# Optimization experiments

Hardware: AMD Instinct MI355X
Metric: run time of the kernel (lower is better)

The kernel has to match this reference:

```python
import jax, jax.numpy as jnp
import numpy as np

H = 768      # hidden_size
R = 64       # lora_dim
E = 8        # n_experts
B, S = 8, 2048


def setup_inputs() -> dict:
    key = jax.random.key(0)
    ks = jax.random.split(key, 10)
    s_in = 1.0 / np.sqrt(H)
    s_r = 1.0 / np.sqrt(R)
    return {
        "x": jax.random.normal(ks[0], (B, S, H), dtype=jnp.float32),
        "enc_w": jax.random.uniform(ks[1], (H, R), jnp.float32, -s_in, s_in),
        "enc_b": jax.random.uniform(ks[2], (R,), jnp.float32, -s_in, s_in),
        "sw_w": jax.random.uniform(ks[3], (R, E), jnp.float32, -s_r, s_r),
        "sw_b": jax.random.uniform(ks[4], (E,), jnp.float32, -s_r, s_r),
        "w1": jax.random.uniform(ks[5], (E, H, R), jnp.float32, -s_in, s_in),
        "b1": jax.random.uniform(ks[6], (E, R), jnp.float32, -s_in, s_in),
        "w2": jax.random.uniform(ks[7], (E, R, H), jnp.float32, -s_r, s_r),
        "b2": jax.random.uniform(ks[8], (E, H), jnp.float32, -s_r, s_r),
    }


def reference(x, enc_w, enc_b, sw_w, sw_b, w1, b1, w2, b2):
    b, s, d = x.shape
    xt = x.reshape(-1, d)                                  # [T, H]
    # router: encoder -> switch -> softmax -> top-1
    x_enc = xt @ enc_w + enc_b                             # [T, R]
    route_prob = jax.nn.softmax(x_enc @ sw_w + sw_b, axis=-1)  # [T, E]
    route_prob_max = jnp.max(route_prob, axis=-1)          # [T]
    routes = jnp.argmax(route_prob, axis=-1)               # [T]
    onehot = jax.nn.one_hot(routes, E, dtype=xt.dtype)     # [T, E]
    # dense dispatch: per-(token, expert) LoRA bottleneck; masked combine
    h = jnp.einsum('td,edr->ter', xt, w1) + b1[None]       # [T, E, R]
    h = jax.nn.gelu(h, approximate=False)
    h = h * onehot[..., None]                              # zero non-routed
    out = jnp.einsum('ter,erd->td', h, w2) + onehot @ b2   # [T, H]
    out = out * route_prob_max[:, None]
    return out.reshape(b, s, d)
```

## Files before the change

kernel.cpp:

```cpp
#include <hip/hip_runtime.h>
#include <math.h>

#define HDIM 768
#define RDIM 64
#define NEXP 8
#define NTOK 16384

typedef _Float16 half8 __attribute__((ext_vector_type(8)));
typedef float float4_t __attribute__((ext_vector_type(4)));

__device__ __forceinline__ float gelu_exact(float v) {
    return 0.5f * v * (1.0f + erff(v * 0.70710678118654752440f));
}

__global__ __launch_bounds__(256) void prep_kernel(
    const float* __restrict__ w1, const float* __restrict__ w2,
    const float* __restrict__ enc_w,
    _Float16* __restrict__ w1t, _Float16* __restrict__ w2t,
    _Float16* __restrict__ enc_hi, _Float16* __restrict__ enc_lo)
{
    const int wid = blockIdx.x * 4 + (threadIdx.x >> 6);
    const int lane = threadIdx.x & 63;
    if (wid < 768) {
        const int e = wid / 96, k0 = (wid % 96) * 8;
        half8 o;
        #pragma unroll
        for (int j = 0; j < 8; j++)
            o[j] = (_Float16)w1[((size_t)(e * HDIM + k0 + j)) * RDIM + lane];
        *(half8*)(w1t + ((size_t)(e * RDIM + lane)) * HDIM + k0) = o;
    } else if (wid < 1536) {
        const int id = wid - 768;
        const int e = id / 96, rem = id % 96;
        const int n = (rem >> 3) * 64 + lane, k0 = (rem & 7) * 8;
        half8 o;
        #pragma unroll
        for (int j = 0; j < 8; j++)
            o[j] = (_Float16)w2[((size_t)(e * RDIM + k0 + j)) * HDIM + n];
        *(half8*)(w2t + ((size_t)(e * HDIM + n)) * RDIM + k0) = o;
    } else if (wid < 1632) {
        const int k0 = (wid - 1536) * 8;
        half8 hi, lo;
        #pragma unroll
        for (int j = 0; j < 8; j++) {
            float v = enc_w[(size_t)(k0 + j) * RDIM + lane];
            _Float16 h = (_Float16)v;
            hi[j] = h;
            lo[j] = (_Float16)(v - (float)h);
        }
        *(half8*)(enc_hi + (size_t)lane * HDIM + k0) = hi;
        *(half8*)(enc_lo + (size_t)lane * HDIM + k0) = lo;
    }
}

__global__ __launch_bounds__(256) void router_kernel(
    const float* __restrict__ x,
    const _Float16* __restrict__ enc_hi, const _Float16* __restrict__ enc_lo,
    const float* __restrict__ enc_b, const float* __restrict__ sw_w,
    const float* __restrict__ sw_b, float* __restrict__ pmax,
    int* __restrict__ counts, int* __restrict__ lists)
{
    __shared__ __align__(16) float xe[64][68];
    __shared__ __align__(16) float sws[512];
    __shared__ int lcnt[NEXP], gbase[NEXP];

    const int tid = threadIdx.x;
    const int tok0 = blockIdx.x * 64;
    const int wv = tid >> 6, lane = tid & 63;
    const int q = lane >> 4, c = lane & 15;

    if (tid < 128) ((float4*)sws)[tid] = ((const float4*)sw_w)[tid];
    if (tid < NEXP) lcnt[tid] = 0;

    const float* xrow = x + (size_t)(tok0 + wv * 16 + c) * HDIM;
    const _Float16* ebase_hi = enc_hi + (size_t)c * HDIM + q * 8;
    const _Float16* ebase_lo = enc_lo + (size_t)c * HDIM + q * 8;

    float4_t acc[4] = {{0,0,0,0},{0,0,0,0},{0,0,0,0},{0,0,0,0}};
    #pragma unroll 2
    for (int k0 = 0; k0 < HDIM; k0 += 32) {
        float4 u0 = *(const float4*)(xrow + k0 + q * 8);
        float4 u1 = *(const float4*)(xrow + k0 + q * 8 + 4);
        float u[8] = {u0.x, u0.y, u0.z, u0.w, u1.x, u1.y, u1.z, u1.w};
        half8 ah, al;
        #pragma unroll
        for (int j = 0; j < 8; j++) {
            _Float16 h = (_Float16)u[j];
            ah[j] = h;
            al[j] = (_Float16)(u[j] - (float)h);
        }
        #pragma unroll
        for (int nf = 0; nf < 4; nf++) {
            half8 bh = *(const half8*)(ebase_hi + (size_t)nf * 16 * HDIM + k0);
            half8 bl = *(const half8*)(ebase_lo + (size_t)nf * 16 * HDIM + k0);
            acc[nf] = __builtin_amdgcn_mfma_f32_16x16x32_f16(ah, bh, acc[nf], 0, 0, 0);
            acc[nf] = __builtin_amdgcn_mfma_f32_16x16x32_f16(ah, bl, acc[nf], 0, 0, 0);
            acc[nf] = __builtin_amdgcn_mfma_f32_16x16x32_f16(al, bh, acc[nf], 0, 0, 0);
        }
    }

    {
        float ebv[4];
        #pragma unroll
        for (int nf = 0; nf < 4; nf++) ebv[nf] = enc_b[nf * 16 + c];
        #pragma unroll
        for (int nf = 0; nf < 4; nf++)
            #pragma unroll
            for (int i = 0; i < 4; i++)
                xe[wv * 16 + q * 4 + i][nf * 16 + c] = acc[nf][i] + ebv[nf];
    }
    __syncthreads();

    int amr[2], lpr[2];
    const int e = tid & 7;
    #pragma unroll
    for (int pass = 0; pass < 2; pass++) {
        const int t = (tid >> 3) + 32 * pass;
        float logit = sw_b[e];
        #pragma unroll 16
        for (int r = 0; r < RDIM; r++)
            logit += xe[t][r] * sws[r * NEXP + e];
        float m = logit; int am = e;
        #pragma unroll
        for (int d = 4; d >= 1; d >>= 1) {
            float om = __shfl_xor(m, d, 8);
            int oam  = __shfl_xor(am, d, 8);
            if (om > m || (om == m && oam < am)) { m = om; am = oam; }
        }
        float s = expf(logit - m);
        #pragma unroll
        for (int d = 1; d <= 4; d <<= 1) s += __shfl_xor(s, d, 8);
        amr[pass] = am; lpr[pass] = 0;
        if (e == 0) {
            pmax[tok0 + t] = 1.0f / s;
            lpr[pass] = atomicAdd(&lcnt[am], 1);
        }
    }
    __syncthreads();
    if (tid < NEXP) gbase[tid] = atomicAdd(&counts[tid * 32], lcnt[tid]);
    __syncthreads();
    if (e == 0) {
        #pragma unroll
        for (int pass = 0; pass < 2; pass++) {
            const int t = (tid >> 3) + 32 * pass;
            lists[amr[pass] * NTOK + gbase[amr[pass]] + lpr[pass]] = tok0 + t;
        }
    }
}

__global__ __launch_bounds__(256) void mm1_kernel(
    const float* __restrict__ x, const _Float16* __restrict__ w1t,
    const float* __restrict__ b1, const int* __restrict__ counts,
    const int* __restrict__ lists, _Float16* __restrict__ h)
{
    const int e = blockIdx.x;
    const int cnt = counts[e * 32];
    const int wv = threadIdx.x >> 6, lane = threadIdx.x & 63;
    const int q = lane >> 4, c = lane & 15;

    for (int st = blockIdx.y * 4 + wv; st * 16 < cnt; st += 512) {
        const int base = st * 16;
        const int nt = cnt - base;
        const int tA = lists[e * NTOK + base + min(c, nt - 1)];
        const float* xrow = x + (size_t)tA * HDIM;
        const _Float16* wbase = w1t + ((size_t)(e * RDIM + c)) * HDIM + q * 8;

        float4_t acc[4] = {{0,0,0,0},{0,0,0,0},{0,0,0,0},{0,0,0,0}};
        #pragma unroll 4
        for (int k0 = 0; k0 < HDIM; k0 += 32) {
            float4 u0 = *(const float4*)(xrow + k0 + q * 8);
            float4 u1 = *(const float4*)(xrow + k0 + q * 8 + 4);
            half8 a;
            a[0] = (_Float16)u0.x; a[1] = (_Float16)u0.y;
            a[2] = (_Float16)u0.z; a[3] = (_Float16)u0.w;
            a[4] = (_Float16)u1.x; a[5] = (_Float16)u1.y;
            a[6] = (_Float16)u1.z; a[7] = (_Float16)u1.w;
            #pragma unroll
            for (int nf = 0; nf < 4; nf++) {
                half8 b = *(const half8*)(wbase + (size_t)nf * 16 * HDIM + k0);
                acc[nf] = __builtin_amdgcn_mfma_f32_16x16x32_f16(a, b, acc[nf], 0, 0, 0);
            }
        }

        #pragma unroll
        for (int i = 0; i < 4; i++) {
            const int row = q * 4 + i;
            if (row < nt) {
                const int tok = lists[e * NTOK + base + row];
                _Float16* hrow = h + (size_t)tok * RDIM;
                #pragma unroll
                for (int nf = 0; nf < 4; nf++) {
                    float v = acc[nf][i] + b1[e * RDIM + nf * 16 + c];
                    hrow[nf * 16 + c] = (_Float16)gelu_exact(v);
                }
            }
        }
    }
}

__global__ __launch_bounds__(256) void mm2_kernel(
    const _Float16* __restrict__ h, const _Float16* __restrict__ w2t,
    const float* __restrict__ b2, const float* __restrict__ pmax,
    const int* __restrict__ counts, const int* __restrict__ lists,
    float* __restrict__ out)
{
    const int e = blockIdx.x;
    const int cnt = counts[e * 32];
    const int wv = threadIdx.x >> 6, lane = threadIdx.x & 63;
    const int q = lane >> 4, c = lane & 15;

    const int task = blockIdx.y * 4 + wv;
    const int nch = task % 3;
    const int sidx = task / 3;

    for (int st = sidx; st * 16 < cnt; st += 128) {
        const int base = st * 16;
        const int nt = cnt - base;
        const int tA = lists[e * NTOK + base + min(c, nt - 1)];
        half8 a0 = *(const half8*)(h + (size_t)tA * RDIM + q * 8);
        half8 a1 = *(const half8*)(h + (size_t)tA * RDIM + 32 + q * 8);

        int tokv[4]; float pm[4]; bool ok[4];
        #pragma unroll
        for (int i = 0; i < 4; i++) {
            const int row = q * 4 + i;
            ok[i] = row < nt;
            tokv[i] = lists[e * NTOK + base + min(row, nt - 1)];
            pm[i] = pmax[tokv[i]];
        }

        #pragma unroll 4
        for (int nf = 0; nf < 16; nf++) {
            const int n = nch * 256 + nf * 16 + c;
            const _Float16* wrow = w2t + ((size_t)(e * HDIM + n)) * RDIM;
            half8 b0 = *(const half8*)(wrow + q * 8);
            half8 b1v = *(const half8*)(wrow + 32 + q * 8);
            float4_t acc = {0, 0, 0, 0};
            acc = __builtin_amdgcn_mfma_f32_16x16x32_f16(a0, b0, acc, 0, 0, 0);
            acc = __builtin_amdgcn_mfma_f32_16x16x32_f16(a1, b1v, acc, 0, 0, 0);
            const float b2v = b2[e * HDIM + n];
            #pragma unroll
            for (int i = 0; i < 4; i++) {
                if (ok[i])
                    out[(size_t)tokv[i] * HDIM + n] = (acc[i] + b2v) * pm[i];
            }
        }
    }
}

extern "C" void kernel_launch(void* const* d_in, const int* in_sizes, int n_in,
                              void* d_out, int out_size, void* d_ws, size_t ws_size,
                              hipStream_t stream) {
    const float* x     = (const float*)d_in[0];
    const float* enc_w = (const float*)d_in[1];
    const float* enc_b = (const float*)d_in[2];
    const float* sw_w  = (const float*)d_in[3];
    const float* sw_b  = (const float*)d_in[4];
    const float* w1    = (const float*)d_in[5];
    const float* b1    = (const float*)d_in[6];
    const float* w2    = (const float*)d_in[7];
    const float* b2    = (const float*)d_in[8];
    float* out = (float*)d_out;

    char* p = (char*)d_ws;
    int*      counts = (int*)p;
    float*    pmax   = (float*)(p + 1024);
    int*      lists  = (int*)(p + 1024 + 65536);
    _Float16* enc_hi = (_Float16*)(p + 590848);
    _Float16* enc_lo = (_Float16*)(p + 590848 + 98304);
    _Float16* w1t    = (_Float16*)(p + 590848 + 196608);
    _Float16* w2t    = (_Float16*)(p + 590848 + 196608 + 786432);
    _Float16* h      = (_Float16*)(p + 590848 + 196608 + 1572864);

    hipMemsetAsync(d_ws, 0, 1024, stream);

    hipLaunchKernelGGL(prep_kernel, dim3(408), dim3(256), 0, stream,
                       w1, w2, enc_w, w1t, w2t, enc_hi, enc_lo);
    hipLaunchKernelGGL(router_kernel, dim3(NTOK / 64), dim3(256), 0, stream,
                       x, enc_hi, enc_lo, enc_b, sw_w, sw_b, pmax, counts, lists);
    hipLaunchKernelGGL(mm1_kernel, dim3(NEXP, 128), dim3(256), 0, stream,
                       x, w1t, b1, counts, lists, h);
    hipLaunchKernelGGL(mm2_kernel, dim3(NEXP, 96), dim3(256), 0, stream,
                       h, w2t, b2, pmax, counts, lists, out);
}
```

Before: 220.0 us.

## Split K dimension across waves in router and mm1 with LDS reduction

Router and mm1 kernels now have each of the four waves compute a quarter of the 768-wide K reduction for one 16-token tile, then combine partials through shared memory. The router grid grows fourfold (16 tokens per block), and mm1 blocks handle one tile at a time instead of four independent per-wave tiles. This raises parallelism and shortens each wave's serial MFMA chain, and it also makes the h writes coalesced per row. In exchange it adds an LDS round trip and extra __syncthreads per tile, and the router leaves half its threads idle during the softmax stage.

```diff
diff --git a/kernel.cpp b/kernel.cpp
--- a/kernel.cpp
+++ b/kernel.cpp
@@ -59,34 +59,35 @@
     const float* __restrict__ sw_b, float* __restrict__ pmax,
     int* __restrict__ counts, int* __restrict__ lists)
 {
-    __shared__ __align__(16) float xe[64][68];
+    __shared__ __align__(16) float part[4][16][68];
     __shared__ __align__(16) float sws[512];
     __shared__ int lcnt[NEXP], gbase[NEXP];
 
     const int tid = threadIdx.x;
-    const int tok0 = blockIdx.x * 64;
+    const int tok0 = blockIdx.x * 16;
     const int wv = tid >> 6, lane = tid & 63;
     const int q = lane >> 4, c = lane & 15;
 
     if (tid < 128) ((float4*)sws)[tid] = ((const float4*)sw_w)[tid];
     if (tid < NEXP) lcnt[tid] = 0;
 
-    const float* xrow = x + (size_t)(tok0 + wv * 16 + c) * HDIM;
-    const _Float16* ebase_hi = enc_hi + (size_t)c * HDIM + q * 8;
-    const _Float16* ebase_lo = enc_lo + (size_t)c * HDIM + q * 8;
+    const float* xrow = x + (size_t)(tok0 + c) * HDIM + wv * 192;
+    const _Float16* ebase_hi = enc_hi + (size_t)c * HDIM + wv * 192 + q * 8;
+    const _Float16* ebase_lo = enc_lo + (size_t)c * HDIM + wv * 192 + q * 8;
 
     float4_t acc[4] = {{0,0,0,0},{0,0,0,0},{0,0,0,0},{0,0,0,0}};
-    #pragma unroll 2
-    for (int k0 = 0; k0 < HDIM; k0 += 32) {
+    #pragma unroll
+    for (int it = 0; it < 6; it++) {
+        const int k0 = it * 32;
         float4 u0 = *(const float4*)(xrow + k0 + q * 8);
         float4 u1 = *(const float4*)(xrow + k0 + q * 8 + 4);
         float u[8] = {u0.x, u0.y, u0.z, u0.w, u1.x, u1.y, u1.z, u1.w};
         half8 ah, al;
         #pragma unroll
         for (int j = 0; j < 8; j++) {
-            _Float16 h = (_Float16)u[j];
-            ah[j] = h;
-            al[j] = (_Float16)(u[j] - (float)h);
+            _Float16 hv = (_Float16)u[j];
+            ah[j] = hv;
+            al[j] = (_Float16)(u[j] - (float)hv);
         }
         #pragma unroll
         for (int nf = 0; nf < 4; nf++) {
@@ -98,27 +99,31 @@
         }
     }
 
-    {
-        float ebv[4];
-        #pragma unroll
-        for (int nf = 0; nf < 4; nf++) ebv[nf] = enc_b[nf * 16 + c];
-        #pragma unroll
-        for (int nf = 0; nf < 4; nf++)
-            #pragma unroll
-            for (int i = 0; i < 4; i++)
-                xe[wv * 16 + q * 4 + i][nf * 16 + c] = acc[nf][i] + ebv[nf];
-    }
-    __syncthreads();
-
-    int amr[2], lpr[2];
-    const int e = tid & 7;
     #pragma unroll
-    for (int pass = 0; pass < 2; pass++) {
-        const int t = (tid >> 3) + 32 * pass;
+    for (int nf = 0; nf < 4; nf++)
+        #pragma unroll
+        for (int i = 0; i < 4; i++)
+            part[wv][q * 4 + i][nf * 16 + c] = acc[nf][i];
+    __syncthreads();
+
+    #pragma unroll
+    for (int j = 0; j < 4; j++) {
+        const int idx = tid + 256 * j;
+        const int row = idx >> 6, r = idx & 63;
+        float v = part[0][row][r] + part[1][row][r] + part[2][row][r]
+                + part[3][row][r] + enc_b[r];
+        part[0][row][r] = v;
+    }
+    __syncthreads();
+
+    int am_s = -1, lp_s = 0;
+    if (tid < 128) {
+        const int e = tid & 7;
+        const int t = tid >> 3;
         float logit = sw_b[e];
         #pragma unroll 16
         for (int r = 0; r < RDIM; r++)
-            logit += xe[t][r] * sws[r * NEXP + e];
+            logit += part[0][t][r] * sws[r * NEXP + e];
         float m = logit; int am = e;
         #pragma unroll
         for (int d = 4; d >= 1; d >>= 1) {
@@ -129,22 +134,17 @@
         float s = expf(logit - m);
         #pragma unroll
         for (int d = 1; d <= 4; d <<= 1) s += __shfl_xor(s, d, 8);
-        amr[pass] = am; lpr[pass] = 0;
         if (e == 0) {
             pmax[tok0 + t] = 1.0f / s;
-            lpr[pass] = atomicAdd(&lcnt[am], 1);
+            am_s = am;
+            lp_s = atomicAdd(&lcnt[am], 1);
         }
     }
     __syncthreads();
     if (tid < NEXP) gbase[tid] = atomicAdd(&counts[tid * 32], lcnt[tid]);
     __syncthreads();
-    if (e == 0) {
-        #pragma unroll
-        for (int pass = 0; pass < 2; pass++) {
-            const int t = (tid >> 3) + 32 * pass;
-            lists[amr[pass] * NTOK + gbase[amr[pass]] + lpr[pass]] = tok0 + t;
-        }
-    }
+    if (am_s >= 0)
+        lists[am_s * NTOK + gbase[am_s] + lp_s] = tok0 + (tid >> 3);
 }
 
 __global__ __launch_bounds__(256) void mm1_kernel(
@@ -152,21 +152,25 @@
     const float* __restrict__ b1, const int* __restrict__ counts,
     const int* __restrict__ lists, _Float16* __restrict__ h)
 {
+    __shared__ __align__(16) float part[4][16][68];
+
     const int e = blockIdx.x;
     const int cnt = counts[e * 32];
-    const int wv = threadIdx.x >> 6, lane = threadIdx.x & 63;
+    const int tid = threadIdx.x;
+    const int wv = tid >> 6, lane = tid & 63;
     const int q = lane >> 4, c = lane & 15;
 
-    for (int st = blockIdx.y * 4 + wv; st * 16 < cnt; st += 512) {
+    for (int st = blockIdx.y; st * 16 < cnt; st += gridDim.y) {
         const int base = st * 16;
         const int nt = cnt - base;
         const int tA = lists[e * NTOK + base + min(c, nt - 1)];
-        const float* xrow = x + (size_t)tA * HDIM;
-        const _Float16* wbase = w1t + ((size_t)(e * RDIM + c)) * HDIM + q * 8;
+        const float* xrow = x + (size_t)tA * HDIM + wv * 192;
+        const _Float16* wbase = w1t + ((size_t)(e * RDIM + c)) * HDIM + wv * 192 + q * 8;
 
         float4_t acc[4] = {{0,0,0,0},{0,0,0,0},{0,0,0,0},{0,0,0,0}};
-        #pragma unroll 4
-        for (int k0 = 0; k0 < HDIM; k0 += 32) {
+        #pragma unroll
+        for (int it = 0; it < 6; it++) {
+            const int k0 = it * 32;
             float4 u0 = *(const float4*)(xrow + k0 + q * 8);
             float4 u1 = *(const float4*)(xrow + k0 + q * 8 + 4);
             half8 a;
@@ -182,18 +186,24 @@
         }
 
         #pragma unroll
-        for (int i = 0; i < 4; i++) {
-            const int row = q * 4 + i;
+        for (int nf = 0; nf < 4; nf++)
+            #pragma unroll
+            for (int i = 0; i < 4; i++)
+                part[wv][q * 4 + i][nf * 16 + c] = acc[nf][i];
+        __syncthreads();
+
+        #pragma unroll
+        for (int j = 0; j < 4; j++) {
+            const int idx = tid + 256 * j;
+            const int row = idx >> 6, r = idx & 63;
             if (row < nt) {
                 const int tok = lists[e * NTOK + base + row];
-                _Float16* hrow = h + (size_t)tok * RDIM;
-                #pragma unroll
-                for (int nf = 0; nf < 4; nf++) {
-                    float v = acc[nf][i] + b1[e * RDIM + nf * 16 + c];
-                    hrow[nf * 16 + c] = (_Float16)gelu_exact(v);
-                }
+                float v = part[0][row][r] + part[1][row][r] + part[2][row][r]
+                        + part[3][row][r] + b1[e * RDIM + r];
+                h[(size_t)tok * RDIM + r] = (_Float16)gelu_exact(v);
             }
         }
+        __syncthreads();
     }
 }
 
@@ -275,7 +285,7 @@
 
     hipLaunchKernelGGL(prep_kernel, dim3(408), dim3(256), 0, stream,
                        w1, w2, enc_w, w1t, w2t, enc_hi, enc_lo);
-    hipLaunchKernelGGL(router_kernel, dim3(NTOK / 64), dim3(256), 0, stream,
+    hipLaunchKernelGGL(router_kernel, dim3(NTOK / 16), dim3(256), 0, stream,
                        x, enc_hi, enc_lo, enc_b, sw_w, sw_b, pmax, counts, lists);
     hipLaunchKernelGGL(mm1_kernel, dim3(NEXP, 128), dim3(256), 0, stream,
                        x, w1t, b1, counts, lists, h);
```

Result: faster. 206.1 us (-6.3%).
